# Kernel tuning notes

Hardware: AMD Instinct MI355X
Metric: run time of the kernel (lower is better)

Reference implementation:

```python
import jax, jax.numpy as jnp
import numpy as np

B, N, D = 4, 2048, 1024
H = 16
DH = D // H  # 64
SCALE = DH ** -0.5


def setup_inputs() -> dict:
    key = jax.random.key(0)
    k1, k2, k3 = jax.random.split(key, 3)
    x = jax.random.normal(k1, (B, N, D), dtype=jnp.float32)
    W_qkv = jax.random.normal(k2, (D, 3 * D), dtype=jnp.float32) / np.sqrt(D)
    b_qkv = jnp.zeros((3 * D,), dtype=jnp.float32)
    W_out = jax.random.normal(k3, (D, D), dtype=jnp.float32) / np.sqrt(D)
    b_out = jnp.zeros((D,), dtype=jnp.float32)
    return {"x": x, "W_qkv": W_qkv, "b_qkv": b_qkv, "W_out": W_out, "b_out": b_out}


def reference(x, W_qkv, b_qkv, W_out, b_out):
    b, n, f = x.shape
    # fused QKV projection: [b, n, 3*D] -> [3, b, H, n, DH]
    qkv = (x @ W_qkv + b_qkv).reshape(b, n, 3, H, DH).transpose(2, 0, 3, 1, 4)
    q, k, v = qkv[0], qkv[1], qkv[2]
    # scaled dot-product attention (dropout rate is 0.0 -> identity)
    attn = jnp.einsum("bhqd,bhkd->bhqk", q, k) * SCALE
    attn = jax.nn.softmax(attn, axis=-1)
    out = jnp.einsum("bhqk,bhkd->bhqd", attn, v)  # [b, H, n, DH]
    out = out.transpose(0, 2, 1, 3).reshape(b, n, f)
    return out @ W_out + b_out
```

## Files before the change

kernel.cpp:

```cpp
#include <hip/hip_runtime.h>
#include <hip/hip_bf16.h>

typedef __bf16 bf16x8 __attribute__((ext_vector_type(8)));
typedef float f32x4 __attribute__((ext_vector_type(4)));
typedef unsigned short u16x8 __attribute__((ext_vector_type(8)));

__device__ inline unsigned short f2bf(float f) {
  __hip_bfloat16 h = __float2bfloat16(f);
  return __builtin_bit_cast(unsigned short, h);
}

__device__ inline f32x4 zero4() {
  f32x4 z;
  #pragma unroll
  for (int i = 0; i < 4; ++i) z[i] = 0.0f;
  return z;
}

__global__ __launch_bounds__(256) void cast_x_kernel(const float* __restrict__ in,
                                                     unsigned short* __restrict__ out, int n4) {
  int i = blockIdx.x * 256 + threadIdx.x;
  if (i < n4) {
    float4 v = ((const float4*)in)[i];
    ushort4 o;
    o.x = f2bf(v.x); o.y = f2bf(v.y); o.z = f2bf(v.z); o.w = f2bf(v.w);
    ((ushort4*)out)[i] = o;
  }
}

__global__ __launch_bounds__(256) void transpose_cast_kernel(const float* __restrict__ in,
                                                             unsigned short* __restrict__ out,
                                                             int R, int C) {
  __shared__ float tile[32][33];
  int c0 = blockIdx.x * 32, r0 = blockIdx.y * 32;
  int tx = threadIdx.x, ty = threadIdx.y;
  #pragma unroll
  for (int i = 0; i < 4; i++)
    tile[ty + i * 8][tx] = in[(size_t)(r0 + ty + i * 8) * C + c0 + tx];
  __syncthreads();
  #pragma unroll
  for (int i = 0; i < 4; i++)
    out[(size_t)(c0 + ty + i * 8) * R + r0 + tx] = f2bf(tile[tx][ty + i * 8]);
}

__global__ __launch_bounds__(256) void transpose_v_kernel(const unsigned short* __restrict__ V,
                                                          unsigned short* __restrict__ Vt) {
  __shared__ unsigned short tile[32][33];
  int k0 = blockIdx.x * 32, d0 = blockIdx.y * 32, bh = blockIdx.z;
  int tx = threadIdx.x, ty = threadIdx.y;
  #pragma unroll
  for (int i = 0; i < 4; i++)
    tile[ty + i * 8][tx] = V[((size_t)bh * 2048 + k0 + ty + i * 8) * 64 + d0 + tx];
  __syncthreads();
  #pragma unroll
  for (int i = 0; i < 4; i++)
    Vt[((size_t)bh * 64 + d0 + ty + i * 8) * 2048 + k0 + tx] = tile[tx][ty + i * 8];
}

template <int KDIM>
__device__ inline void gemm_tile(const unsigned short* __restrict__ A,
                                 const unsigned short* __restrict__ BT,
                                 int m0, int n0,
                                 unsigned short* ldsA, unsigned short* ldsB,
                                 f32x4 acc[4][4]) {
  const int t = threadIdx.x;
  const int lane = t & 63;
  const int w = t >> 6;
  const int wm = w >> 1, wn = w & 1;
  const int fr = lane & 15;
  const int fg = lane >> 4;

  #pragma unroll
  for (int m = 0; m < 4; m++)
    #pragma unroll
    for (int n = 0; n < 4; n++) acc[m][n] = zero4();

  for (int kt = 0; kt < KDIM / 64; ++kt) {
    #pragma unroll
    for (int p = 0; p < 4; p++) {
      int c = t + p * 256;
      int row = c >> 3, cc = c & 7;
      *(u16x8*)(ldsA + row * 72 + cc * 8) =
          *(const u16x8*)(A + (size_t)(m0 + row) * KDIM + kt * 64 + cc * 8);
      *(u16x8*)(ldsB + row * 72 + cc * 8) =
          *(const u16x8*)(BT + (size_t)(n0 + row) * KDIM + kt * 64 + cc * 8);
    }
    __syncthreads();
    #pragma unroll
    for (int ks = 0; ks < 2; ++ks) {
      bf16x8 a[4], b[4];
      #pragma unroll
      for (int m = 0; m < 4; m++)
        a[m] = *(const bf16x8*)(ldsA + (wm * 64 + m * 16 + fr) * 72 + ks * 32 + fg * 8);
      #pragma unroll
      for (int n = 0; n < 4; n++)
        b[n] = *(const bf16x8*)(ldsB + (wn * 64 + n * 16 + fr) * 72 + ks * 32 + fg * 8);
      #pragma unroll
      for (int m = 0; m < 4; m++)
        #pragma unroll
        for (int n = 0; n < 4; n++)
          acc[m][n] = __builtin_amdgcn_mfma_f32_16x16x32_bf16(a[m], b[n], acc[m][n], 0, 0, 0);
    }
    __syncthreads();
  }
}

__global__ __launch_bounds__(256) void gemm_qkv_kernel(const unsigned short* __restrict__ xbf,
                                                       const unsigned short* __restrict__ WqkvT,
                                                       const float* __restrict__ bqkv,
                                                       unsigned short* __restrict__ Qws,
                                                       unsigned short* __restrict__ Kws,
                                                       unsigned short* __restrict__ Vws) {
  __shared__ unsigned short ldsA[128 * 72];
  __shared__ unsigned short ldsB[128 * 72];
  int m0 = blockIdx.y * 128, n0 = blockIdx.x * 128;
  f32x4 acc[4][4];
  gemm_tile<1024>(xbf, WqkvT, m0, n0, ldsA, ldsB, acc);

  const int lane = threadIdx.x & 63;
  const int w = threadIdx.x >> 6;
  const int wm = w >> 1, wn = w & 1;
  const int fr = lane & 15, fg = lane >> 4;
  #pragma unroll
  for (int m = 0; m < 4; m++) {
    #pragma unroll
    for (int n = 0; n < 4; n++) {
      int col = n0 + wn * 64 + n * 16 + fr;
      int s = col >> 10, h = (col >> 6) & 15, d = col & 63;
      float bias = bqkv[col];
      float sc = (s == 0) ? 0.125f : 1.0f;
      unsigned short* dst = (s == 0) ? Qws : ((s == 1) ? Kws : Vws);
      #pragma unroll
      for (int r = 0; r < 4; r++) {
        int row = m0 + wm * 64 + m * 16 + fg * 4 + r;
        int bb = row >> 11, tok = row & 2047;
        dst[((size_t)(bb * 16 + h) * 2048 + tok) * 64 + d] = f2bf((acc[m][n][r] + bias) * sc);
      }
    }
  }
}

__global__ __launch_bounds__(256) void attn_kernel(const unsigned short* __restrict__ Qws,
                                                   const unsigned short* __restrict__ Kws,
                                                   const unsigned short* __restrict__ Vtws,
                                                   unsigned short* __restrict__ attn_out) {
  __shared__ unsigned short ldsK[64 * 72];
  __shared__ unsigned short ldsV[64 * 72];
  const int t = threadIdx.x, lane = t & 63, w = t >> 6;
  const int bh = blockIdx.x >> 4, qt = blockIdx.x & 15;
  const int q0 = qt * 128;
  const int fr = lane & 15, fg = lane >> 4;
  const size_t bhbase = (size_t)bh * 2048;

  bf16x8 qf[2][2];
  #pragma unroll
  for (int u = 0; u < 2; u++) {
    const unsigned short* qrow = Qws + (bhbase + q0 + w * 32 + u * 16 + fr) * 64;
    qf[u][0] = *(const bf16x8*)(qrow + fg * 8);
    qf[u][1] = *(const bf16x8*)(qrow + 32 + fg * 8);
  }

  float m_run[2] = {-1e30f, -1e30f}, l_run[2] = {0.0f, 0.0f};
  f32x4 ot[2][4];
  #pragma unroll
  for (int u = 0; u < 2; u++)
    #pragma unroll
    for (int dt = 0; dt < 4; dt++) ot[u][dt] = zero4();

  int kslot[2];
  #pragma unroll
  for (int p = 0; p < 2; p++) {
    int kk = (t + p * 256) >> 3;
    int w32 = kk & 31;
    kslot[p] = ((kk >> 5) * 2 + ((w32 >> 2) & 1)) * 16 + ((w32 >> 3) << 2) + (w32 & 3);
  }

  for (int kb = 0; kb < 2048; kb += 64) {
    u16x8 kreg[2], vreg[2];
    #pragma unroll
    for (int p = 0; p < 2; p++) {
      int c = t + p * 256;
      int row = c >> 3, cc = c & 7;
      kreg[p] = *(const u16x8*)(Kws + (bhbase + kb + row) * 64 + cc * 8);
      vreg[p] = *(const u16x8*)(Vtws + ((size_t)bh * 64 + row) * 2048 + kb + cc * 8);
    }
    __syncthreads();
    #pragma unroll
    for (int p = 0; p < 2; p++) {
      int c = t + p * 256;
      int row = c >> 3, cc = c & 7;
      *(u16x8*)(ldsK + kslot[p] * 72 + cc * 8) = kreg[p];
      *(u16x8*)(ldsV + row * 72 + cc * 8) = vreg[p];
    }
    __syncthreads();

    f32x4 st[2][4];
    #pragma unroll
    for (int c = 0; c < 4; c++) {
      bf16x8 a0 = *(const bf16x8*)(ldsK + (c * 16 + fr) * 72 + fg * 8);
      bf16x8 a1 = *(const bf16x8*)(ldsK + (c * 16 + fr) * 72 + 32 + fg * 8);
      #pragma unroll
      for (int u = 0; u < 2; u++) {
        st[u][c] = __builtin_amdgcn_mfma_f32_16x16x32_bf16(a0, qf[u][0], zero4(), 0, 0, 0);
        st[u][c] = __builtin_amdgcn_mfma_f32_16x16x32_bf16(a1, qf[u][1], st[u][c], 0, 0, 0);
      }
    }

    u16x8 pb[2][2];
    #pragma unroll
    for (int u = 0; u < 2; u++) {
      float tmax = -1e30f;
      #pragma unroll
      for (int c = 0; c < 4; c++)
        #pragma unroll
        for (int r = 0; r < 4; r++) tmax = fmaxf(tmax, st[u][c][r]);
      tmax = fmaxf(tmax, __shfl_xor(tmax, 16, 64));
      tmax = fmaxf(tmax, __shfl_xor(tmax, 32, 64));
      float m_new = fmaxf(m_run[u], tmax);
      float corr = __expf(m_run[u] - m_new);
      float tsum = 0.0f;
      #pragma unroll
      for (int c = 0; c < 4; c++)
        #pragma unroll
        for (int r = 0; r < 4; r++) {
          st[u][c][r] = __expf(st[u][c][r] - m_new);
          tsum += st[u][c][r];
        }
      tsum += __shfl_xor(tsum, 16, 64);
      tsum += __shfl_xor(tsum, 32, 64);
      l_run[u] = l_run[u] * corr + tsum;
      m_run[u] = m_new;
      #pragma unroll
      for (int dt = 0; dt < 4; dt++) ot[u][dt] *= corr;

      #pragma unroll
      for (int kc = 0; kc < 2; kc++) {
        u16x8 v;
        #pragma unroll
        for (int j = 0; j < 4; j++) {
          v[j] = f2bf(st[u][kc * 2][j]);
          v[4 + j] = f2bf(st[u][kc * 2 + 1][j]);
        }
        pb[u][kc] = v;
      }
    }

    #pragma unroll
    for (int dt = 0; dt < 4; dt++) {
      #pragma unroll
      for (int kc = 0; kc < 2; kc++) {
        bf16x8 av = *(const bf16x8*)(ldsV + (dt * 16 + fr) * 72 + kc * 32 + fg * 8);
        #pragma unroll
        for (int u = 0; u < 2; u++)
          ot[u][dt] = __builtin_amdgcn_mfma_f32_16x16x32_bf16(
              av, __builtin_bit_cast(bf16x8, pb[u][kc]), ot[u][dt], 0, 0, 0);
      }
    }
  }

  const int b = bh >> 4, h = bh & 15;
  #pragma unroll
  for (int u = 0; u < 2; u++) {
    float rl = 1.0f / l_run[u];
    int q = q0 + w * 32 + u * 16 + fr;
    #pragma unroll
    for (int dt = 0; dt < 4; dt++) {
      ushort4 o;
      o.x = f2bf(ot[u][dt][0] * rl);
      o.y = f2bf(ot[u][dt][1] * rl);
      o.z = f2bf(ot[u][dt][2] * rl);
      o.w = f2bf(ot[u][dt][3] * rl);
      int d = dt * 16 + fg * 4;
      *(ushort4*)(attn_out + ((size_t)b * 2048 + q) * 1024 + h * 64 + d) = o;
    }
  }
}

__global__ __launch_bounds__(256) void gemm_out_kernel(const unsigned short* __restrict__ attn,
                                                       const unsigned short* __restrict__ WoutT,
                                                       const float* __restrict__ bout,
                                                       float* __restrict__ out) {
  __shared__ unsigned short ldsA[128 * 72];
  __shared__ unsigned short ldsB[128 * 72];
  int m0 = blockIdx.y * 128, n0 = blockIdx.x * 128;
  f32x4 acc[4][4];
  gemm_tile<1024>(attn, WoutT, m0, n0, ldsA, ldsB, acc);

  const int lane = threadIdx.x & 63;
  const int w = threadIdx.x >> 6;
  const int wm = w >> 1, wn = w & 1;
  const int fr = lane & 15, fg = lane >> 4;
  #pragma unroll
  for (int m = 0; m < 4; m++) {
    #pragma unroll
    for (int n = 0; n < 4; n++) {
      int col = n0 + wn * 64 + n * 16 + fr;
      float bias = bout[col];
      #pragma unroll
      for (int r = 0; r < 4; r++) {
        int row = m0 + wm * 64 + m * 16 + fg * 4 + r;
        out[(size_t)row * 1024 + col] = acc[m][n][r] + bias;
      }
    }
  }
}

extern "C" void kernel_launch(void* const* d_in, const int* in_sizes, int n_in,
                              void* d_out, int out_size, void* d_ws, size_t ws_size,
                              hipStream_t stream) {
  const float* x = (const float*)d_in[0];
  const float* Wqkv = (const float*)d_in[1];
  const float* bqkv = (const float*)d_in[2];
  const float* Wout = (const float*)d_in[3];
  const float* bout = (const float*)d_in[4];
  float* out = (float*)d_out;

  unsigned short* xbf = (unsigned short*)d_ws;
  unsigned short* wqkvT = xbf + 8388608;
  unsigned short* woutT = wqkvT + 3145728;
  unsigned short* Qws = woutT + 1048576;
  unsigned short* Kws = Qws + 8388608;
  unsigned short* Vws = Kws + 8388608;
  unsigned short* Vtws = Vws + 8388608;
  unsigned short* attn = xbf;

  cast_x_kernel<<<2097152 / 256, 256, 0, stream>>>(x, xbf, 2097152);
  transpose_cast_kernel<<<dim3(96, 32), dim3(32, 8), 0, stream>>>(Wqkv, wqkvT, 1024, 3072);
  transpose_cast_kernel<<<dim3(32, 32), dim3(32, 8), 0, stream>>>(Wout, woutT, 1024, 1024);
  gemm_qkv_kernel<<<dim3(24, 64), 256, 0, stream>>>(xbf, wqkvT, bqkv, Qws, Kws, Vws);
  transpose_v_kernel<<<dim3(64, 2, 64), dim3(32, 8), 0, stream>>>(Vws, Vtws);
  attn_kernel<<<1024, 256, 0, stream>>>(Qws, Kws, Vtws, attn);
  gemm_out_kernel<<<dim3(8, 64), 256, 0, stream>>>(attn, woutT, bout, out);
}
```

Baseline: 324.8 us.

## Use direct global-to-LDS loads, pre-swizzled K/V tiles, double buffering, lazy softmax rescale

GEMM tiles and attention K/V tiles now go straight from global memory into LDS via global_load_lds, which removes the register staging round trip. K and V are written by the producer kernels in a pre-swizzled, tile-contiguous layout so reads need no padding and avoid bank conflicts. The attention kernel double-buffers K/V and remaps blocks across heads. Softmax switches to exp2 with log2e folded into the Q scale, and skips the output rescale unless the max grows by more than a threshold. This adds layout coupling between kernels and depends on the async load and single-barrier ordering being correct.

```diff
diff --git a/kernel.cpp b/kernel.cpp
--- a/kernel.cpp
+++ b/kernel.cpp
@@ -16,6 +16,14 @@
   for (int i = 0; i < 4; ++i) z[i] = 0.0f;
   return z;
 }
+
+__device__ inline void gload16(const unsigned short* g, unsigned short* l) {
+  __builtin_amdgcn_global_load_lds(
+      (const __attribute__((address_space(1))) unsigned int*)g,
+      (__attribute__((address_space(3))) unsigned int*)l, 16, 0, 0);
+}
+
+#define QSCALE 0.18033688011112042f
 
 __global__ __launch_bounds__(256) void cast_x_kernel(const float* __restrict__ in,
                                                      unsigned short* __restrict__ out, int n4) {
@@ -44,17 +52,22 @@
 }
 
 __global__ __launch_bounds__(256) void transpose_v_kernel(const unsigned short* __restrict__ V,
-                                                          unsigned short* __restrict__ Vt) {
-  __shared__ unsigned short tile[32][33];
+                                                          unsigned short* __restrict__ Vst) {
+  __shared__ unsigned short tl[32][33];
   int k0 = blockIdx.x * 32, d0 = blockIdx.y * 32, bh = blockIdx.z;
   int tx = threadIdx.x, ty = threadIdx.y;
   #pragma unroll
   for (int i = 0; i < 4; i++)
-    tile[ty + i * 8][tx] = V[((size_t)bh * 2048 + k0 + ty + i * 8) * 64 + d0 + tx];
+    tl[ty + i * 8][tx] = V[((size_t)bh * 2048 + k0 + ty + i * 8) * 64 + d0 + tx];
   __syncthreads();
   #pragma unroll
-  for (int i = 0; i < 4; i++)
-    Vt[((size_t)bh * 64 + d0 + ty + i * 8) * 2048 + k0 + tx] = tile[tx][ty + i * 8];
+  for (int i = 0; i < 4; i++) {
+    int dd = d0 + ty + i * 8;
+    int tok = k0 + tx;
+    int tile = tok >> 6, k = tok & 63;
+    Vst[((size_t)bh * 32 + tile) * 4096 + dd * 64 + (((k >> 3) ^ (dd & 7)) * 8) + (k & 7)] =
+        tl[tx][ty + i * 8];
+  }
 }
 
 template <int KDIM>
@@ -69,6 +82,8 @@
   const int wm = w >> 1, wn = w & 1;
   const int fr = lane & 15;
   const int fg = lane >> 4;
+  const int srow = w * 8 + (lane >> 3);
+  const int scol = (lane & 7) * 8;
 
   #pragma unroll
   for (int m = 0; m < 4; m++)
@@ -76,14 +91,12 @@
     for (int n = 0; n < 4; n++) acc[m][n] = zero4();
 
   for (int kt = 0; kt < KDIM / 64; ++kt) {
-    #pragma unroll
-    for (int p = 0; p < 4; p++) {
-      int c = t + p * 256;
-      int row = c >> 3, cc = c & 7;
-      *(u16x8*)(ldsA + row * 72 + cc * 8) =
-          *(const u16x8*)(A + (size_t)(m0 + row) * KDIM + kt * 64 + cc * 8);
-      *(u16x8*)(ldsB + row * 72 + cc * 8) =
-          *(const u16x8*)(BT + (size_t)(n0 + row) * KDIM + kt * 64 + cc * 8);
+    __syncthreads();
+    #pragma unroll
+    for (int i = 0; i < 4; i++) {
+      int row = i * 32 + srow;
+      gload16(A + (size_t)(m0 + row) * KDIM + kt * 64 + scol, ldsA + row * 64 + scol);
+      gload16(BT + (size_t)(n0 + row) * KDIM + kt * 64 + scol, ldsB + row * 64 + scol);
     }
     __syncthreads();
     #pragma unroll
@@ -91,17 +104,16 @@
       bf16x8 a[4], b[4];
       #pragma unroll
       for (int m = 0; m < 4; m++)
-        a[m] = *(const bf16x8*)(ldsA + (wm * 64 + m * 16 + fr) * 72 + ks * 32 + fg * 8);
+        a[m] = *(const bf16x8*)(ldsA + (wm * 64 + m * 16 + fr) * 64 + ks * 32 + fg * 8);
       #pragma unroll
       for (int n = 0; n < 4; n++)
-        b[n] = *(const bf16x8*)(ldsB + (wn * 64 + n * 16 + fr) * 72 + ks * 32 + fg * 8);
+        b[n] = *(const bf16x8*)(ldsB + (wn * 64 + n * 16 + fr) * 64 + ks * 32 + fg * 8);
       #pragma unroll
       for (int m = 0; m < 4; m++)
         #pragma unroll
         for (int n = 0; n < 4; n++)
           acc[m][n] = __builtin_amdgcn_mfma_f32_16x16x32_bf16(a[m], b[n], acc[m][n], 0, 0, 0);
     }
-    __syncthreads();
   }
 }
 
@@ -109,10 +121,10 @@
                                                        const unsigned short* __restrict__ WqkvT,
                                                        const float* __restrict__ bqkv,
                                                        unsigned short* __restrict__ Qws,
-                                                       unsigned short* __restrict__ Kws,
+                                                       unsigned short* __restrict__ Kst,
                                                        unsigned short* __restrict__ Vws) {
-  __shared__ unsigned short ldsA[128 * 72];
-  __shared__ unsigned short ldsB[128 * 72];
+  __shared__ unsigned short ldsA[128 * 64];
+  __shared__ unsigned short ldsB[128 * 64];
   int m0 = blockIdx.y * 128, n0 = blockIdx.x * 128;
   f32x4 acc[4][4];
   gemm_tile<1024>(xbf, WqkvT, m0, n0, ldsA, ldsB, acc);
@@ -126,30 +138,42 @@
     #pragma unroll
     for (int n = 0; n < 4; n++) {
       int col = n0 + wn * 64 + n * 16 + fr;
-      int s = col >> 10, h = (col >> 6) & 15, d = col & 63;
+      int s = col >> 10, cc = col & 1023, h = cc >> 6, d = cc & 63;
       float bias = bqkv[col];
-      float sc = (s == 0) ? 0.125f : 1.0f;
-      unsigned short* dst = (s == 0) ? Qws : ((s == 1) ? Kws : Vws);
       #pragma unroll
       for (int r = 0; r < 4; r++) {
         int row = m0 + wm * 64 + m * 16 + fg * 4 + r;
         int bb = row >> 11, tok = row & 2047;
-        dst[((size_t)(bb * 16 + h) * 2048 + tok) * 64 + d] = f2bf((acc[m][n][r] + bias) * sc);
+        int bh = bb * 16 + h;
+        float val = acc[m][n][r] + bias;
+        if (s == 0) {
+          Qws[((size_t)bh * 2048 + tok) * 64 + d] = f2bf(val * QSCALE);
+        } else if (s == 1) {
+          int kk = tok & 63, tile = tok >> 6;
+          int w32 = kk & 31;
+          int sg = ((kk >> 5) * 2 + ((w32 >> 2) & 1)) * 16 + ((w32 >> 3) << 2) + (w32 & 3);
+          Kst[((size_t)bh * 32 + tile) * 4096 + sg * 64 + (((d >> 3) ^ (sg & 7)) * 8) + (d & 7)] =
+              f2bf(val);
+        } else {
+          Vws[((size_t)bh * 2048 + tok) * 64 + d] = f2bf(val);
+        }
       }
     }
   }
 }
 
 __global__ __launch_bounds__(256) void attn_kernel(const unsigned short* __restrict__ Qws,
-                                                   const unsigned short* __restrict__ Kws,
-                                                   const unsigned short* __restrict__ Vtws,
+                                                   const unsigned short* __restrict__ Kst,
+                                                   const unsigned short* __restrict__ Vst,
                                                    unsigned short* __restrict__ attn_out) {
-  __shared__ unsigned short ldsK[64 * 72];
-  __shared__ unsigned short ldsV[64 * 72];
+  __shared__ unsigned short ldsK[2][4096];
+  __shared__ unsigned short ldsV[2][4096];
   const int t = threadIdx.x, lane = t & 63, w = t >> 6;
-  const int bh = blockIdx.x >> 4, qt = blockIdx.x & 15;
+  int bid = blockIdx.x;
+  int vid = (bid & 7) * 128 + (bid >> 3);
+  const int bh = vid >> 4, qt = vid & 15;
   const int q0 = qt * 128;
-  const int fr = lane & 15, fg = lane >> 4;
+  const int fr = lane & 15, fg = lane >> 4, sw = fr & 7;
   const size_t bhbase = (size_t)bh * 2048;
 
   bf16x8 qf[2][2];
@@ -167,38 +191,36 @@
     #pragma unroll
     for (int dt = 0; dt < 4; dt++) ot[u][dt] = zero4();
 
-  int kslot[2];
-  #pragma unroll
-  for (int p = 0; p < 2; p++) {
-    int kk = (t + p * 256) >> 3;
-    int w32 = kk & 31;
-    kslot[p] = ((kk >> 5) * 2 + ((w32 >> 2) & 1)) * 16 + ((w32 >> 3) << 2) + (w32 & 3);
-  }
-
-  for (int kb = 0; kb < 2048; kb += 64) {
-    u16x8 kreg[2], vreg[2];
-    #pragma unroll
-    for (int p = 0; p < 2; p++) {
-      int c = t + p * 256;
-      int row = c >> 3, cc = c & 7;
-      kreg[p] = *(const u16x8*)(Kws + (bhbase + kb + row) * 64 + cc * 8);
-      vreg[p] = *(const u16x8*)(Vtws + ((size_t)bh * 64 + row) * 2048 + kb + cc * 8);
-    }
+  const unsigned short* kbase = Kst + (size_t)bh * 32 * 4096 + w * 1024 + lane * 8;
+  const unsigned short* vbase = Vst + (size_t)bh * 32 * 4096 + w * 1024 + lane * 8;
+  unsigned short* kl = &ldsK[0][0] + w * 1024 + lane * 8;
+  unsigned short* vl = &ldsV[0][0] + w * 1024 + lane * 8;
+
+  {
+    gload16(kbase, kl);           gload16(kbase + 512, kl + 512);
+    gload16(vbase, vl);           gload16(vbase + 512, vl + 512);
+  }
+
+  int cur = 0;
+  for (int tt = 0; tt < 32; ++tt) {
     __syncthreads();
-    #pragma unroll
-    for (int p = 0; p < 2; p++) {
-      int c = t + p * 256;
-      int row = c >> 3, cc = c & 7;
-      *(u16x8*)(ldsK + kslot[p] * 72 + cc * 8) = kreg[p];
-      *(u16x8*)(ldsV + row * 72 + cc * 8) = vreg[p];
-    }
-    __syncthreads();
+    if (tt + 1 < 32) {
+      const unsigned short* kg = kbase + (size_t)(tt + 1) * 4096;
+      const unsigned short* vg = vbase + (size_t)(tt + 1) * 4096;
+      unsigned short* kd = kl + (cur ^ 1) * 4096;
+      unsigned short* vd = vl + (cur ^ 1) * 4096;
+      gload16(kg, kd);            gload16(kg + 512, kd + 512);
+      gload16(vg, vd);            gload16(vg + 512, vd + 512);
+    }
+    const unsigned short* Kb = &ldsK[cur][0];
+    const unsigned short* Vb = &ldsV[cur][0];
 
     f32x4 st[2][4];
     #pragma unroll
     for (int c = 0; c < 4; c++) {
-      bf16x8 a0 = *(const bf16x8*)(ldsK + (c * 16 + fr) * 72 + fg * 8);
-      bf16x8 a1 = *(const bf16x8*)(ldsK + (c * 16 + fr) * 72 + 32 + fg * 8);
+      const unsigned short* krow = Kb + (c * 16 + fr) * 64;
+      bf16x8 a0 = *(const bf16x8*)(krow + ((fg ^ sw) * 8));
+      bf16x8 a1 = *(const bf16x8*)(krow + (((4 + fg) ^ sw) * 8));
       #pragma unroll
       for (int u = 0; u < 2; u++) {
         st[u][c] = __builtin_amdgcn_mfma_f32_16x16x32_bf16(a0, qf[u][0], zero4(), 0, 0, 0);
@@ -209,29 +231,32 @@
     u16x8 pb[2][2];
     #pragma unroll
     for (int u = 0; u < 2; u++) {
-      float tmax = -1e30f;
+      float tmax = st[u][0][0];
       #pragma unroll
       for (int c = 0; c < 4; c++)
         #pragma unroll
         for (int r = 0; r < 4; r++) tmax = fmaxf(tmax, st[u][c][r]);
       tmax = fmaxf(tmax, __shfl_xor(tmax, 16, 64));
       tmax = fmaxf(tmax, __shfl_xor(tmax, 32, 64));
-      float m_new = fmaxf(m_run[u], tmax);
-      float corr = __expf(m_run[u] - m_new);
+      if (!__all(tmax <= m_run[u] + 11.0f)) {
+        float m_new = fmaxf(m_run[u], tmax);
+        float corr = exp2f(m_run[u] - m_new);
+        l_run[u] *= corr;
+        #pragma unroll
+        for (int dt = 0; dt < 4; dt++) ot[u][dt] *= corr;
+        m_run[u] = m_new;
+      }
       float tsum = 0.0f;
       #pragma unroll
       for (int c = 0; c < 4; c++)
         #pragma unroll
         for (int r = 0; r < 4; r++) {
-          st[u][c][r] = __expf(st[u][c][r] - m_new);
+          st[u][c][r] = exp2f(st[u][c][r] - m_run[u]);
           tsum += st[u][c][r];
         }
       tsum += __shfl_xor(tsum, 16, 64);
       tsum += __shfl_xor(tsum, 32, 64);
-      l_run[u] = l_run[u] * corr + tsum;
-      m_run[u] = m_new;
-      #pragma unroll
-      for (int dt = 0; dt < 4; dt++) ot[u][dt] *= corr;
+      l_run[u] += tsum;
 
       #pragma unroll
       for (int kc = 0; kc < 2; kc++) {
@@ -247,15 +272,17 @@
 
     #pragma unroll
     for (int dt = 0; dt < 4; dt++) {
+      const unsigned short* vrow = Vb + (dt * 16 + fr) * 64;
       #pragma unroll
       for (int kc = 0; kc < 2; kc++) {
-        bf16x8 av = *(const bf16x8*)(ldsV + (dt * 16 + fr) * 72 + kc * 32 + fg * 8);
+        bf16x8 av = *(const bf16x8*)(vrow + (((kc * 4 + fg) ^ sw) * 8));
         #pragma unroll
         for (int u = 0; u < 2; u++)
           ot[u][dt] = __builtin_amdgcn_mfma_f32_16x16x32_bf16(
               av, __builtin_bit_cast(bf16x8, pb[u][kc]), ot[u][dt], 0, 0, 0);
       }
     }
+    cur ^= 1;
   }
 
   const int b = bh >> 4, h = bh & 15;
@@ -280,8 +307,8 @@
                                                        const unsigned short* __restrict__ WoutT,
                                                        const float* __restrict__ bout,
                                                        float* __restrict__ out) {
-  __shared__ unsigned short ldsA[128 * 72];
-  __shared__ unsigned short ldsB[128 * 72];
+  __shared__ unsigned short ldsA[128 * 64];
+  __shared__ unsigned short ldsB[128 * 64];
   int m0 = blockIdx.y * 128, n0 = blockIdx.x * 128;
   f32x4 acc[4][4];
   gemm_tile<1024>(attn, WoutT, m0, n0, ldsA, ldsB, acc);
@@ -319,16 +346,16 @@
   unsigned short* wqkvT = xbf + 8388608;
   unsigned short* woutT = wqkvT + 3145728;
   unsigned short* Qws = woutT + 1048576;
-  unsigned short* Kws = Qws + 8388608;
-  unsigned short* Vws = Kws + 8388608;
-  unsigned short* Vtws = Vws + 8388608;
+  unsigned short* Kst = Qws + 8388608;
+  unsigned short* Vws = Kst + 8388608;
+  unsigned short* Vst = Vws + 8388608;
   unsigned short* attn = xbf;
 
-  cast_x_kernel<<<2097152 / 256, 256, 0, stream>>>(x, xbf, 2097152);
+  cast_x_kernel<<<8192, 256, 0, stream>>>(x, xbf, 2097152);
   transpose_cast_kernel<<<dim3(96, 32), dim3(32, 8), 0, stream>>>(Wqkv, wqkvT, 1024, 3072);
   transpose_cast_kernel<<<dim3(32, 32), dim3(32, 8), 0, stream>>>(Wout, woutT, 1024, 1024);
-  gemm_qkv_kernel<<<dim3(24, 64), 256, 0, stream>>>(xbf, wqkvT, bqkv, Qws, Kws, Vws);
-  transpose_v_kernel<<<dim3(64, 2, 64), dim3(32, 8), 0, stream>>>(Vws, Vtws);
-  attn_kernel<<<1024, 256, 0, stream>>>(Qws, Kws, Vtws, attn);
+  gemm_qkv_kernel<<<dim3(24, 64), 256, 0, stream>>>(xbf, wqkvT, bqkv, Qws, Kst, Vws);
+  transpose_v_kernel<<<dim3(64, 2, 64), dim3(32, 8), 0, stream>>>(Vws, Vst);
+  attn_kernel<<<1024, 256, 0, stream>>>(Qws, Kst, Vst, attn);
   gemm_out_kernel<<<dim3(8, 64), 256, 0, stream>>>(attn, woutT, bout, out);
 }
```

Result: slower. 346.6 us (+6.7%).
